# Performance work log

Measured on AMD Instinct MI355X. Metric: run time of the kernel, lower is better.

Reference implementation:

```python
import jax, jax.numpy as jnp
import numpy as np

N0, N1, N2 = 819200, 81920, 8192
E1, E2 = 819200, 81920
DIN, DH, DOUT = 128, 256, 128


def setup_inputs() -> dict:
    key = jax.random.key(0)
    ks = jax.random.split(key, 12)
    inp = {
        "x": jax.random.normal(ks[0], (N0, DIN), dtype=jnp.float32),
        "src1": jax.random.randint(ks[1], (E1,), 0, N0, dtype=jnp.int32),
        "dst1": jax.random.randint(ks[2], (E1,), 0, N1, dtype=jnp.int32),
        "src2": jax.random.randint(ks[3], (E2,), 0, N1, dtype=jnp.int32),
        "dst2": jax.random.randint(ks[4], (E2,), 0, N2, dtype=jnp.int32),
        "n1": N1,
        "n2": N2,
        # SAGEConv layer 1 params (lin_l has bias, lin_r no bias, PyG default)
        "w1l": jax.random.normal(ks[5], (DIN, DH), dtype=jnp.float32) / np.sqrt(DIN),
        "b1": jnp.zeros((DH,), dtype=jnp.float32),
        "w1r": jax.random.normal(ks[6], (DIN, DH), dtype=jnp.float32) / np.sqrt(DIN),
        # SAGEConv layer 2 params
        "w2l": jax.random.normal(ks[7], (DH, DOUT), dtype=jnp.float32) / np.sqrt(DH),
        "b2": jnp.zeros((DOUT,), dtype=jnp.float32),
        "w2r": jax.random.normal(ks[8], (DH, DOUT), dtype=jnp.float32) / np.sqrt(DH),
    }
    return inp


def _sage_conv(x_src, x_dst, src, dst, n_dst, wl, bl, wr):
    # mean aggregation of neighbor (source) features into destinations
    msg = x_src[src]                                            # [E, d]
    agg = jax.ops.segment_sum(msg, dst, num_segments=n_dst)     # [n_dst, d]
    cnt = jax.ops.segment_sum(jnp.ones((dst.shape[0],), msg.dtype), dst,
                              num_segments=n_dst)               # [n_dst]
    mean = agg / jnp.maximum(cnt, 1.0)[:, None]
    return mean @ wl + bl + x_dst @ wr


def reference(x, src1, dst1, src2, dst2, n1, n2, w1l, b1, w1r, w2l, b2, w2r):
    # layer 1 (eval mode: dropout is a no-op)
    h = _sage_conv(x, x[:n1], src1, dst1, n1, w1l, b1, w1r)     # [n1, DH]
    h = jax.nn.relu(h)
    # layer 2
    out = _sage_conv(h, h[:n2], src2, dst2, n2, w2l, b2, w2r)   # [n2, DOUT]
    return out
```

## Files before the change

kernel.cpp:

```cpp
#include <hip/hip_runtime.h>

constexpr int cN0 = 819200, cN1 = 81920, cN2 = 8192;
constexpr int cE1 = 819200, cE2 = 81920;
constexpr int cEtot = cE1 + cE2;
constexpr int cDIN = 128, cDH = 256, cDOUT = 128;
constexpr int cNOFF = cN1 + cN2;
constexpr int cSBLK = 88;

typedef __attribute__((ext_vector_type(8))) short bf16x8;
typedef __attribute__((ext_vector_type(4))) float f32x4;
typedef __attribute__((ext_vector_type(8))) unsigned short u16x8;

__device__ __forceinline__ unsigned short f2bf(float f) {
    unsigned u = __builtin_bit_cast(unsigned, f);
    u += 0x7FFF + ((u >> 16) & 1);
    return (unsigned short)(u >> 16);
}
__device__ __forceinline__ float bf2f(unsigned short s) {
    unsigned u = ((unsigned)s) << 16;
    return __builtin_bit_cast(float, u);
}

#define GLOAD_LDS16(g, l) __builtin_amdgcn_global_load_lds(               \
    (const __attribute__((address_space(1))) void*)(g),                   \
    (__attribute__((address_space(3))) void*)(l), 16, 0, 0)

__global__ __launch_bounds__(256) void setup2_k(
    int* __restrict__ offs,
    const int* __restrict__ dst1, const int* __restrict__ dst2,
    const float* __restrict__ w1l, const float* __restrict__ w1r,
    const float* __restrict__ w2l, const float* __restrict__ w2r,
    unsigned short* __restrict__ W1c, unsigned short* __restrict__ W2c,
    const float* __restrict__ x, unsigned short* __restrict__ xb)
{
    int id = blockIdx.x * 256 + threadIdx.x;
    if (id < cEtot) {
        if (id < cE1) atomicAdd(&offs[dst1[id]], 1);
        else atomicAdd(&offs[cN1 + dst2[id - cE1]], 1);
        return;
    }
    id -= cEtot;
    if (id < 256 * 256) {
        int n = id >> 8, k = id & 255;
        float v = (k < 128) ? w1l[k * 256 + n] : w1r[(k - 128) * 256 + n];
        W1c[n * 256 + k] = f2bf(v);
        return;
    }
    id -= 256 * 256;
    if (id < 128 * 512) {
        int n = id >> 9, k = id & 511;
        float v = (k < 256) ? w2l[k * 128 + n] : w2r[(k - 256) * 128 + n];
        W2c[n * 512 + k] = f2bf(v);
        return;
    }
    id -= 128 * 512;
    {
        const float* p = x + (size_t)id * 8;
        float4 a = *reinterpret_cast<const float4*>(p);
        float4 b = *reinterpret_cast<const float4*>(p + 4);
        u16x8 o;
        o[0] = f2bf(a.x); o[1] = f2bf(a.y); o[2] = f2bf(a.z); o[3] = f2bf(a.w);
        o[4] = f2bf(b.x); o[5] = f2bf(b.y); o[6] = f2bf(b.z); o[7] = f2bf(b.w);
        reinterpret_cast<u16x8*>(xb)[id] = o;
    }
}

__global__ __launch_bounds__(1024) void scan_lb_k(
    int* __restrict__ a, unsigned* __restrict__ word)
{
    const int tid = threadIdx.x, bid = blockIdx.x;
    const int lane = tid & 63, wid = tid >> 6;
    const int g = bid * 1024 + tid;
    __shared__ int ws[16];
    __shared__ int aggs[cSBLK];
    __shared__ int pex[cSBLK];
    __shared__ int sh_excl;

    int v = a[g];
    int incl = v;
    #pragma unroll
    for (int off = 1; off < 64; off <<= 1) {
        int t = __shfl_up(incl, off, 64);
        if (lane >= off) incl += t;
    }
    if (lane == 63) ws[wid] = incl;
    __syncthreads();
    int wpre = 0;
    #pragma unroll
    for (int w = 0; w < 15; ++w) if (w < wid) wpre += ws[w];
    const int lexcl = wpre + incl - v;
    if (tid == 0) {
        int tot = 0;
        #pragma unroll
        for (int w = 0; w < 16; ++w) tot += ws[w];
        __hip_atomic_store(&word[bid], ((unsigned)tot << 2) | 1u,
                           __ATOMIC_RELEASE, __HIP_MEMORY_SCOPE_AGENT);
    }

    if (bid == 0) {
        if (tid < cSBLK) {
            unsigned wv;
            do {
                wv = __hip_atomic_load(&word[tid], __ATOMIC_ACQUIRE,
                                       __HIP_MEMORY_SCOPE_AGENT);
            } while ((wv & 3u) == 0u);
            aggs[tid] = (int)(wv >> 2);
        }
        __syncthreads();
        if (tid == 0) {
            int run = 0;
            for (int i = 0; i < cSBLK; ++i) { pex[i] = run; run += aggs[i]; }
        }
        __syncthreads();
        if (tid < cSBLK)
            __hip_atomic_store(&word[tid], ((unsigned)pex[tid] << 2) | 2u,
                               __ATOMIC_RELEASE, __HIP_MEMORY_SCOPE_AGENT);
    }

    if (tid == 0) {
        unsigned wv;
        do {
            wv = __hip_atomic_load(&word[bid], __ATOMIC_ACQUIRE,
                                   __HIP_MEMORY_SCOPE_AGENT);
        } while ((wv & 3u) != 2u);
        sh_excl = (int)(wv >> 2);
    }
    __syncthreads();
    int r = sh_excl + lexcl;
    if (g >= cN1) r -= cE1;
    a[g] = r;
}

__global__ __launch_bounds__(256) void build_k(
    const int* __restrict__ src1, const int* __restrict__ dst1,
    const int* __restrict__ src2, const int* __restrict__ dst2,
    int* __restrict__ offs, int* __restrict__ eidx1, int* __restrict__ eidx2)
{
    int e = blockIdx.x * 256 + threadIdx.x;
    if (e < cE1) {
        int p = atomicAdd(&offs[dst1[e]], 1);
        eidx1[p] = src1[e];
    } else {
        int e2 = e - cE1;
        if (e2 < cE2) {
            int p = atomicAdd(&offs[cN1 + dst2[e2]], 1);
            eidx2[p] = src2[e2];
        }
    }
}

__global__ __launch_bounds__(256) void agg1_k(
    const float* __restrict__ x, const int* __restrict__ cursor,
    const int* __restrict__ eidx, unsigned short* __restrict__ mean1)
{
    const int row = blockIdx.x * 4 + (threadIdx.x >> 6);
    const int lane = threadIdx.x & 63;
    const int g = lane >> 4, li = lane & 15;
    const int start = row ? cursor[row - 1] : 0;
    const int end = cursor[row];
    float acc[8] = {};
    for (int e = start + g; e < end; e += 4) {
        const int s = eidx[e];
        const float4* p = reinterpret_cast<const float4*>(x + (size_t)s * cDIN + li * 8);
        float4 a = p[0], b = p[1];
        acc[0] += a.x; acc[1] += a.y; acc[2] += a.z; acc[3] += a.w;
        acc[4] += b.x; acc[5] += b.y; acc[6] += b.z; acc[7] += b.w;
    }
    #pragma unroll
    for (int i = 0; i < 8; ++i) {
        acc[i] += __shfl_xor(acc[i], 16);
        acc[i] += __shfl_xor(acc[i], 32);
    }
    if (g == 0) {
        const float inv = 1.0f / fmaxf((float)(end - start), 1.0f);
        u16x8 o;
        #pragma unroll
        for (int i = 0; i < 8; ++i) o[i] = f2bf(acc[i] * inv);
        *reinterpret_cast<u16x8*>(mean1 + (size_t)row * cDIN + li * 8) = o;
    }
}

__global__ __launch_bounds__(256) void agg2_k(
    const unsigned short* __restrict__ h, const int* __restrict__ cursor,
    const int* __restrict__ eidx, unsigned short* __restrict__ mean2)
{
    const int row = blockIdx.x * 4 + (threadIdx.x >> 6);
    const int lane = threadIdx.x & 63;
    const int g = lane >> 4, li = lane & 15;
    const int start = row ? cursor[row - 1] : 0;
    const int end = cursor[row];
    float acc[16] = {};
    for (int e = start + g; e < end; e += 4) {
        const int s = eidx[e];
        const u16x8* p = reinterpret_cast<const u16x8*>(h + (size_t)s * cDH + li * 16);
        u16x8 a = p[0], b = p[1];
        #pragma unroll
        for (int i = 0; i < 8; ++i) { acc[i] += bf2f(a[i]); acc[8 + i] += bf2f(b[i]); }
    }
    #pragma unroll
    for (int i = 0; i < 16; ++i) {
        acc[i] += __shfl_xor(acc[i], 16);
        acc[i] += __shfl_xor(acc[i], 32);
    }
    if (g == 0) {
        const float inv = 1.0f / fmaxf((float)(end - start), 1.0f);
        u16x8 o0, o1;
        #pragma unroll
        for (int i = 0; i < 8; ++i) { o0[i] = f2bf(acc[i] * inv); o1[i] = f2bf(acc[8 + i] * inv); }
        u16x8* q = reinterpret_cast<u16x8*>(mean2 + (size_t)row * cDH + li * 16);
        q[0] = o0; q[1] = o1;
    }
}

__global__ __launch_bounds__(256) void gemm1_k(
    const unsigned short* __restrict__ mean1,
    const unsigned short* __restrict__ xb,
    const unsigned short* __restrict__ W1c,
    const float* __restrict__ b1,
    unsigned short* __restrict__ h)
{
    __shared__ unsigned short As[128 * 32];
    __shared__ unsigned short Bs[128 * 32];

    const int tid = threadIdx.x;
    const int l = tid & 63, w = tid >> 6;
    const int q = l >> 4, r16 = l & 15;
    const int wr0 = (w >> 1) * 64, wc0 = (w & 1) * 64;
    const int n0 = blockIdx.x * 128, row0 = blockIdx.y * 128;

    const int srow = w * 32 + (l >> 2);
    const int skoff = (l & 3) * 8;

    const f32x4 zero = {0.f, 0.f, 0.f, 0.f};
    f32x4 acc[4][4];
    #pragma unroll
    for (int m = 0; m < 4; ++m)
        #pragma unroll
        for (int n = 0; n < 4; ++n) acc[m][n] = zero;

    for (int k0 = 0; k0 < 256; k0 += 32) {
        const unsigned short* Asrc = (k0 < 128) ? mean1 : xb;
        const int kk = k0 & 127;
        __syncthreads();
        #pragma unroll
        for (int j = 0; j < 2; ++j) {
            const int r = srow + j * 16;
            GLOAD_LDS16(Asrc + (size_t)(row0 + r) * 128 + kk + skoff,
                        As + (w * 2 + j) * 512);
            GLOAD_LDS16(W1c + (size_t)(n0 + r) * 256 + k0 + skoff,
                        Bs + (w * 2 + j) * 512);
        }
        __syncthreads();
        bf16x8 af[4], bg[4];
        #pragma unroll
        for (int m = 0; m < 4; ++m)
            af[m] = *reinterpret_cast<const bf16x8*>(As + (wr0 + 16 * m + r16) * 32 + q * 8);
        #pragma unroll
        for (int n = 0; n < 4; ++n)
            bg[n] = *reinterpret_cast<const bf16x8*>(Bs + (wc0 + 16 * n + r16) * 32 + q * 8);
        #pragma unroll
        for (int m = 0; m < 4; ++m)
            #pragma unroll
            for (int n = 0; n < 4; ++n)
                acc[m][n] = __builtin_amdgcn_mfma_f32_16x16x32_bf16(af[m], bg[n], acc[m][n], 0, 0, 0);
    }

    #pragma unroll
    for (int n = 0; n < 4; ++n) {
        const int col = n0 + wc0 + 16 * n + r16;
        const float bv = b1[col];
        #pragma unroll
        for (int m = 0; m < 4; ++m) {
            #pragma unroll
            for (int j = 0; j < 4; ++j) {
                const int row = row0 + wr0 + 16 * m + 4 * q + j;
                h[(size_t)row * cDH + col] = f2bf(fmaxf(acc[m][n][j] + bv, 0.f));
            }
        }
    }
}

__global__ __launch_bounds__(256) void gemm2_k(
    const unsigned short* __restrict__ mean2,
    const unsigned short* __restrict__ hd,
    const unsigned short* __restrict__ W2c,
    const float* __restrict__ b2, float* __restrict__ out)
{
    constexpr int K = 512, KL = 256, N = 128, TM = 32;
    constexpr int LD = 40;
    __shared__ unsigned short As[TM * LD];
    __shared__ unsigned short Bs[128 * LD];

    const int tid = threadIdx.x;
    const int l = tid & 63, w = tid >> 6;
    const int q = l >> 4, r16 = l & 15;
    const int wc0 = w * 32;
    const int row0 = blockIdx.y * TM;

    const f32x4 zero = {0.f, 0.f, 0.f, 0.f};
    f32x4 acc[2][2];
    acc[0][0] = zero; acc[0][1] = zero; acc[1][0] = zero; acc[1][1] = zero;

    for (int k0 = 0; k0 < K; k0 += 32) {
        const bool left = (k0 < KL);
        const unsigned short* Asrc = left ? mean2 : hd;
        const int kk = k0 & (KL - 1);
        __syncthreads();
        if (tid < TM * 4) {
            int r = tid >> 2, o16 = tid & 3;
            bf16x8 av = *reinterpret_cast<const bf16x8*>(Asrc + (size_t)(row0 + r) * KL + kk + o16 * 8);
            *reinterpret_cast<bf16x8*>(As + r * LD + o16 * 8) = av;
        }
        #pragma unroll
        for (int c = 0; c < 2; ++c) {
            int z = tid + c * 256;
            int r = z >> 2, o16 = z & 3;
            bf16x8 bv = *reinterpret_cast<const bf16x8*>(W2c + (size_t)r * K + k0 + o16 * 8);
            *reinterpret_cast<bf16x8*>(Bs + r * LD + o16 * 8) = bv;
        }
        __syncthreads();
        bf16x8 af[2], bg[2];
        #pragma unroll
        for (int m = 0; m < 2; ++m)
            af[m] = *reinterpret_cast<const bf16x8*>(As + (16 * m + r16) * LD + q * 8);
        #pragma unroll
        for (int n = 0; n < 2; ++n)
            bg[n] = *reinterpret_cast<const bf16x8*>(Bs + (wc0 + 16 * n + r16) * LD + q * 8);
        #pragma unroll
        for (int m = 0; m < 2; ++m)
            #pragma unroll
            for (int n = 0; n < 2; ++n)
                acc[m][n] = __builtin_amdgcn_mfma_f32_16x16x32_bf16(af[m], bg[n], acc[m][n], 0, 0, 0);
    }

    #pragma unroll
    for (int n = 0; n < 2; ++n) {
        const int col = wc0 + 16 * n + r16;
        const float bv = b2[col];
        #pragma unroll
        for (int m = 0; m < 2; ++m) {
            #pragma unroll
            for (int j = 0; j < 4; ++j) {
                const int row = row0 + 16 * m + 4 * q + j;
                out[(size_t)row * N + col] = acc[m][n][j] + bv;
            }
        }
    }
}

extern "C" void kernel_launch(void* const* d_in, const int* in_sizes, int n_in,
                              void* d_out, int out_size, void* d_ws, size_t ws_size,
                              hipStream_t stream)
{
    const float* x    = (const float*)d_in[0];
    const int*   src1 = (const int*)d_in[1];
    const int*   dst1 = (const int*)d_in[2];
    const int*   src2 = (const int*)d_in[3];
    const int*   dst2 = (const int*)d_in[4];
    const float* w1l  = (const float*)d_in[7];
    const float* b1   = (const float*)d_in[8];
    const float* w1r  = (const float*)d_in[9];
    const float* w2l  = (const float*)d_in[10];
    const float* b2   = (const float*)d_in[11];
    const float* w2r  = (const float*)d_in[12];
    float* out = (float*)d_out;

    unsigned short* mean1 = (unsigned short*)d_ws;
    unsigned short* h     = mean1 + (size_t)cN1 * cDIN;
    unsigned short* mean2 = h + (size_t)cN1 * cDH;
    unsigned short* W1c   = mean2 + (size_t)cN2 * cDH;
    unsigned short* W2c   = W1c + 256 * 256;
    unsigned short* xb    = W2c + 128 * 512;
    int* offs  = (int*)(xb + (size_t)cN1 * cDIN);
    unsigned* word = (unsigned*)(offs + cNOFF);
    int* eidx1 = (int*)(word + cSBLK);
    int* eidx2 = eidx1 + cE1;

    hipMemsetAsync(offs, 0, (size_t)(cNOFF + cSBLK) * sizeof(int), stream);
    {
        int total = cEtot + 256 * 256 + 128 * 512 + cN1 * cDIN / 8;
        setup2_k<<<total / 256, 256, 0, stream>>>(offs, dst1, dst2,
                                                  w1l, w1r, w2l, w2r,
                                                  W1c, W2c, x, xb);
    }
    scan_lb_k<<<cSBLK, 1024, 0, stream>>>(offs, word);
    build_k<<<(cE1 + cE2) / 256, 256, 0, stream>>>(src1, dst1, src2, dst2, offs, eidx1, eidx2);
    agg1_k<<<cN1 / 4, 256, 0, stream>>>(x, offs, eidx1, mean1);
    gemm1_k<<<dim3(2, cN1 / 128), 256, 0, stream>>>(mean1, xb, W1c, b1, h);
    agg2_k<<<cN2 / 4, 256, 0, stream>>>(h, offs + cN1, eidx2, mean2);
    gemm2_k<<<dim3(1, cN2 / 32), 256, 0, stream>>>(mean2, h, W2c, b2, out);
}
```

Baseline: 242.7 us.

## Fuse mean aggregation into the layer GEMM kernels via shared-memory tiles

Merges agg1 with gemm1 and agg2 with gemm2. Each block first gathers and averages its neighbor rows straight into LDS as bf16 K-slices, then runs the MFMA GEMM reading those slices from LDS, so the mean1 and mean2 global buffers and two kernel launches disappear. Layer 1 now uses 512-thread blocks that cover all 256 output columns, so each A tile is loaded once. The cost is a gather with one 16-lane group walking each row's edges serially instead of four groups splitting them, and higher LDS use per block, which may cut occupancy and memory-level parallelism in the bandwidth-bound gather.

```diff
diff --git a/kernel.cpp b/kernel.cpp
--- a/kernel.cpp
+++ b/kernel.cpp
@@ -149,87 +149,43 @@
     }
 }
 
-__global__ __launch_bounds__(256) void agg1_k(
-    const float* __restrict__ x, const int* __restrict__ cursor,
-    const int* __restrict__ eidx, unsigned short* __restrict__ mean1)
-{
-    const int row = blockIdx.x * 4 + (threadIdx.x >> 6);
-    const int lane = threadIdx.x & 63;
-    const int g = lane >> 4, li = lane & 15;
-    const int start = row ? cursor[row - 1] : 0;
-    const int end = cursor[row];
-    float acc[8] = {};
-    for (int e = start + g; e < end; e += 4) {
-        const int s = eidx[e];
-        const float4* p = reinterpret_cast<const float4*>(x + (size_t)s * cDIN + li * 8);
-        float4 a = p[0], b = p[1];
-        acc[0] += a.x; acc[1] += a.y; acc[2] += a.z; acc[3] += a.w;
-        acc[4] += b.x; acc[5] += b.y; acc[6] += b.z; acc[7] += b.w;
-    }
-    #pragma unroll
-    for (int i = 0; i < 8; ++i) {
-        acc[i] += __shfl_xor(acc[i], 16);
-        acc[i] += __shfl_xor(acc[i], 32);
-    }
-    if (g == 0) {
+__global__ __launch_bounds__(512) void fused1_k(
+    const float* __restrict__ x, const int* __restrict__ offs,
+    const int* __restrict__ eidx, const unsigned short* __restrict__ xb,
+    const unsigned short* __restrict__ W1c, const float* __restrict__ b1,
+    unsigned short* __restrict__ h)
+{
+    __shared__ unsigned short meanS[4][128 * 32];
+    __shared__ unsigned short As[128 * 32];
+    __shared__ unsigned short Bs[256 * 32];
+
+    const int tid = threadIdx.x;
+    const int l = tid & 63, w = tid >> 6;
+    const int g16 = l >> 4, li = l & 15;
+    const int row0 = blockIdx.x * 128;
+
+    for (int rr = g16; rr < 16; rr += 4) {
+        const int lr = 16 * w + rr;
+        const int rowg = row0 + lr;
+        const int start = rowg ? offs[rowg - 1] : 0;
+        const int end = offs[rowg];
+        float acc[8] = {};
+        for (int e = start; e < end; ++e) {
+            const int s = eidx[e];
+            const float4* p = reinterpret_cast<const float4*>(x + (size_t)s * cDIN + li * 8);
+            float4 a = p[0], b = p[1];
+            acc[0] += a.x; acc[1] += a.y; acc[2] += a.z; acc[3] += a.w;
+            acc[4] += b.x; acc[5] += b.y; acc[6] += b.z; acc[7] += b.w;
+        }
         const float inv = 1.0f / fmaxf((float)(end - start), 1.0f);
         u16x8 o;
         #pragma unroll
         for (int i = 0; i < 8; ++i) o[i] = f2bf(acc[i] * inv);
-        *reinterpret_cast<u16x8*>(mean1 + (size_t)row * cDIN + li * 8) = o;
-    }
-}
-
-__global__ __launch_bounds__(256) void agg2_k(
-    const unsigned short* __restrict__ h, const int* __restrict__ cursor,
-    const int* __restrict__ eidx, unsigned short* __restrict__ mean2)
-{
-    const int row = blockIdx.x * 4 + (threadIdx.x >> 6);
-    const int lane = threadIdx.x & 63;
-    const int g = lane >> 4, li = lane & 15;
-    const int start = row ? cursor[row - 1] : 0;
-    const int end = cursor[row];
-    float acc[16] = {};
-    for (int e = start + g; e < end; e += 4) {
-        const int s = eidx[e];
-        const u16x8* p = reinterpret_cast<const u16x8*>(h + (size_t)s * cDH + li * 16);
-        u16x8 a = p[0], b = p[1];
-        #pragma unroll
-        for (int i = 0; i < 8; ++i) { acc[i] += bf2f(a[i]); acc[8 + i] += bf2f(b[i]); }
-    }
-    #pragma unroll
-    for (int i = 0; i < 16; ++i) {
-        acc[i] += __shfl_xor(acc[i], 16);
-        acc[i] += __shfl_xor(acc[i], 32);
-    }
-    if (g == 0) {
-        const float inv = 1.0f / fmaxf((float)(end - start), 1.0f);
-        u16x8 o0, o1;
-        #pragma unroll
-        for (int i = 0; i < 8; ++i) { o0[i] = f2bf(acc[i] * inv); o1[i] = f2bf(acc[8 + i] * inv); }
-        u16x8* q = reinterpret_cast<u16x8*>(mean2 + (size_t)row * cDH + li * 16);
-        q[0] = o0; q[1] = o1;
-    }
-}
-
-__global__ __launch_bounds__(256) void gemm1_k(
-    const unsigned short* __restrict__ mean1,
-    const unsigned short* __restrict__ xb,
-    const unsigned short* __restrict__ W1c,
-    const float* __restrict__ b1,
-    unsigned short* __restrict__ h)
-{
-    __shared__ unsigned short As[128 * 32];
-    __shared__ unsigned short Bs[128 * 32];
-
-    const int tid = threadIdx.x;
-    const int l = tid & 63, w = tid >> 6;
+        *reinterpret_cast<u16x8*>(&meanS[li >> 2][lr * 32 + (li & 3) * 8]) = o;
+    }
+
     const int q = l >> 4, r16 = l & 15;
-    const int wr0 = (w >> 1) * 64, wc0 = (w & 1) * 64;
-    const int n0 = blockIdx.x * 128, row0 = blockIdx.y * 128;
-
-    const int srow = w * 32 + (l >> 2);
-    const int skoff = (l & 3) * 8;
+    const int wr0 = (w >> 2) * 64, wc0 = (w & 3) * 64;
 
     const f32x4 zero = {0.f, 0.f, 0.f, 0.f};
     f32x4 acc[4][4];
@@ -238,23 +194,26 @@
         #pragma unroll
         for (int n = 0; n < 4; ++n) acc[m][n] = zero;
 
-    for (int k0 = 0; k0 < 256; k0 += 32) {
-        const unsigned short* Asrc = (k0 < 128) ? mean1 : xb;
-        const int kk = k0 & 127;
+    for (int kc = 0; kc < 8; ++kc) {
         __syncthreads();
         #pragma unroll
         for (int j = 0; j < 2; ++j) {
-            const int r = srow + j * 16;
-            GLOAD_LDS16(Asrc + (size_t)(row0 + r) * 128 + kk + skoff,
-                        As + (w * 2 + j) * 512);
-            GLOAD_LDS16(W1c + (size_t)(n0 + r) * 256 + k0 + skoff,
-                        Bs + (w * 2 + j) * 512);
-        }
-        __syncthreads();
+            const int z = j * 512 + w * 64 + l;
+            GLOAD_LDS16(W1c + (size_t)(z >> 2) * 256 + kc * 32 + (z & 3) * 8,
+                        Bs + (size_t)z * 8);
+        }
+        if (kc >= 4) {
+            const int z = tid;
+            GLOAD_LDS16(xb + (size_t)(row0 + (z >> 2)) * cDIN + (kc - 4) * 32 + (z & 3) * 8,
+                        As + (size_t)z * 8);
+        }
+        __syncthreads();
+
+        const unsigned short* Asrc = (kc < 4) ? meanS[kc] : As;
         bf16x8 af[4], bg[4];
         #pragma unroll
         for (int m = 0; m < 4; ++m)
-            af[m] = *reinterpret_cast<const bf16x8*>(As + (wr0 + 16 * m + r16) * 32 + q * 8);
+            af[m] = *reinterpret_cast<const bf16x8*>(Asrc + (wr0 + 16 * m + r16) * 32 + q * 8);
         #pragma unroll
         for (int n = 0; n < 4; ++n)
             bg[n] = *reinterpret_cast<const bf16x8*>(Bs + (wc0 + 16 * n + r16) * 32 + q * 8);
@@ -267,7 +226,7 @@
 
     #pragma unroll
     for (int n = 0; n < 4; ++n) {
-        const int col = n0 + wc0 + 16 * n + r16;
+        const int col = wc0 + 16 * n + r16;
         const float bv = b1[col];
         #pragma unroll
         for (int m = 0; m < 4; ++m) {
@@ -280,52 +239,71 @@
     }
 }
 
-__global__ __launch_bounds__(256) void gemm2_k(
-    const unsigned short* __restrict__ mean2,
-    const unsigned short* __restrict__ hd,
-    const unsigned short* __restrict__ W2c,
-    const float* __restrict__ b2, float* __restrict__ out)
-{
-    constexpr int K = 512, KL = 256, N = 128, TM = 32;
-    constexpr int LD = 40;
-    __shared__ unsigned short As[TM * LD];
-    __shared__ unsigned short Bs[128 * LD];
+__global__ __launch_bounds__(256) void fused2_k(
+    const unsigned short* __restrict__ hfull, const int* __restrict__ offs2,
+    const int* __restrict__ eidx, const unsigned short* __restrict__ hd,
+    const unsigned short* __restrict__ W2c, const float* __restrict__ b2,
+    float* __restrict__ out)
+{
+    __shared__ unsigned short meanS[8][32 * 32];
+    __shared__ unsigned short As[32 * 32];
+    __shared__ unsigned short Bs[128 * 32];
 
     const int tid = threadIdx.x;
     const int l = tid & 63, w = tid >> 6;
+    const int g16 = l >> 4, li = l & 15;
+    const int row0 = blockIdx.x * 32;
+
+    for (int rr = w * 4 + g16; rr < 32; rr += 16) {
+        const int rowg = row0 + rr;
+        const int start = rowg ? offs2[rowg - 1] : 0;
+        const int end = offs2[rowg];
+        float acc[16] = {};
+        for (int e = start; e < end; ++e) {
+            const int s = eidx[e];
+            const u16x8* p = reinterpret_cast<const u16x8*>(hfull + (size_t)s * cDH + li * 16);
+            u16x8 a = p[0], b = p[1];
+            #pragma unroll
+            for (int i = 0; i < 8; ++i) { acc[i] += bf2f(a[i]); acc[8 + i] += bf2f(b[i]); }
+        }
+        const float inv = 1.0f / fmaxf((float)(end - start), 1.0f);
+        u16x8 o0, o1;
+        #pragma unroll
+        for (int i = 0; i < 8; ++i) { o0[i] = f2bf(acc[i] * inv); o1[i] = f2bf(acc[8 + i] * inv); }
+        *reinterpret_cast<u16x8*>(&meanS[li >> 1][rr * 32 + (li & 1) * 16 + 0]) = o0;
+        *reinterpret_cast<u16x8*>(&meanS[li >> 1][rr * 32 + (li & 1) * 16 + 8]) = o1;
+    }
+
     const int q = l >> 4, r16 = l & 15;
     const int wc0 = w * 32;
-    const int row0 = blockIdx.y * TM;
 
     const f32x4 zero = {0.f, 0.f, 0.f, 0.f};
     f32x4 acc[2][2];
     acc[0][0] = zero; acc[0][1] = zero; acc[1][0] = zero; acc[1][1] = zero;
 
-    for (int k0 = 0; k0 < K; k0 += 32) {
-        const bool left = (k0 < KL);
-        const unsigned short* Asrc = left ? mean2 : hd;
-        const int kk = k0 & (KL - 1);
-        __syncthreads();
-        if (tid < TM * 4) {
-            int r = tid >> 2, o16 = tid & 3;
-            bf16x8 av = *reinterpret_cast<const bf16x8*>(Asrc + (size_t)(row0 + r) * KL + kk + o16 * 8);
-            *reinterpret_cast<bf16x8*>(As + r * LD + o16 * 8) = av;
-        }
-        #pragma unroll
-        for (int c = 0; c < 2; ++c) {
-            int z = tid + c * 256;
-            int r = z >> 2, o16 = z & 3;
-            bf16x8 bv = *reinterpret_cast<const bf16x8*>(W2c + (size_t)r * K + k0 + o16 * 8);
-            *reinterpret_cast<bf16x8*>(Bs + r * LD + o16 * 8) = bv;
-        }
-        __syncthreads();
+    for (int kc = 0; kc < 16; ++kc) {
+        __syncthreads();
+        #pragma unroll
+        for (int j = 0; j < 2; ++j) {
+            const int z = j * 256 + w * 64 + l;
+            GLOAD_LDS16(W2c + (size_t)(z >> 2) * 512 + kc * 32 + (z & 3) * 8,
+                        Bs + (size_t)z * 8);
+        }
+        if (kc >= 8 && w < 2) {
+            const int z = w * 64 + l;
+            GLOAD_LDS16(hd + (size_t)(row0 + (z >> 2)) * cDH + (kc - 8) * 32 + (z & 3) * 8,
+                        As + (size_t)z * 8);
+        }
+        __syncthreads();
+
+        const unsigned short* Asrc = (kc < 8) ? meanS[kc] : As;
         bf16x8 af[2], bg[2];
         #pragma unroll
         for (int m = 0; m < 2; ++m)
-            af[m] = *reinterpret_cast<const bf16x8*>(As + (16 * m + r16) * LD + q * 8);
+            af[m] = *reinterpret_cast<const bf16x8*>(Asrc + (16 * m + r16) * 32 + q * 8);
         #pragma unroll
         for (int n = 0; n < 2; ++n)
-            bg[n] = *reinterpret_cast<const bf16x8*>(Bs + (wc0 + 16 * n + r16) * LD + q * 8);
+            bg[n] = *reinterpret_cast<const bf16x8*>(Bs + (wc0 + 16 * n + r16) * 32 + q * 8);
         #pragma unroll
         for (int m = 0; m < 2; ++m)
             #pragma unroll
@@ -342,7 +320,7 @@
             #pragma unroll
             for (int j = 0; j < 4; ++j) {
                 const int row = row0 + 16 * m + 4 * q + j;
-                out[(size_t)row * N + col] = acc[m][n][j] + bv;
+                out[(size_t)row * cDOUT + col] = acc[m][n][j] + bv;
             }
         }
     }
@@ -365,12 +343,10 @@
     const float* w2r  = (const float*)d_in[12];
     float* out = (float*)d_out;
 
-    unsigned short* mean1 = (unsigned short*)d_ws;
-    unsigned short* h     = mean1 + (size_t)cN1 * cDIN;
-    unsigned short* mean2 = h + (size_t)cN1 * cDH;
-    unsigned short* W1c   = mean2 + (size_t)cN2 * cDH;
-    unsigned short* W2c   = W1c + 256 * 256;
-    unsigned short* xb    = W2c + 128 * 512;
+    unsigned short* h   = (unsigned short*)d_ws;
+    unsigned short* W1c = h + (size_t)cN1 * cDH;
+    unsigned short* W2c = W1c + 256 * 256;
+    unsigned short* xb  = W2c + 128 * 512;
     int* offs  = (int*)(xb + (size_t)cN1 * cDIN);
     unsigned* word = (unsigned*)(offs + cNOFF);
     int* eidx1 = (int*)(word + cSBLK);
@@ -384,9 +360,7 @@
                                                   W1c, W2c, x, xb);
     }
     scan_lb_k<<<cSBLK, 1024, 0, stream>>>(offs, word);
-    build_k<<<(cE1 + cE2) / 256, 256, 0, stream>>>(src1, dst1, src2, dst2, offs, eidx1, eidx2);
-    agg1_k<<<cN1 / 4, 256, 0, stream>>>(x, offs, eidx1, mean1);
-    gemm1_k<<<dim3(2, cN1 / 128), 256, 0, stream>>>(mean1, xb, W1c, b1, h);
-    agg2_k<<<cN2 / 4, 256, 0, stream>>>(h, offs + cN1, eidx2, mean2);
-    gemm2_k<<<dim3(1, cN2 / 32), 256, 0, stream>>>(mean2, h, W2c, b2, out);
-}
+    build_k<<<cEtot / 256, 256, 0, stream>>>(src1, dst1, src2, dst2, offs, eidx1, eidx2);
+    fused1_k<<<cN1 / 128, 512, 0, stream>>>(x, offs, eidx1, xb, W1c, b1, h);
+    fused2_k<<<cN2 / 32, 256, 0, stream>>>(h, offs + cN1, eidx2, h, W2c, b2, out);
+}
```

Measured after the change: 329.0 us. +35.6%, slower.
